# Performance work log

Hardware: AMD Instinct MI355X
Metric: run time of the kernel (lower is better)

Reference implementation:

```python
import jax, jax.numpy as jnp
import numpy as np

N_NODES = 100000
N_EDGES = 1600000
IN_CH = 128
HID = 64
HEADS = 2
OUT_CH = 2
EDGE_DIM = 3
NEG_SLOPE = 0.2
EPS = 1e-16  # PyG softmax denominator epsilon


def gat_conv(x, edge_index, edge_attr, W, We, att_src, att_dst, att_edge, bias, heads, out_ch, concat):
    """Faithful PyG GATConv (edge_dim enabled, eval mode, add_self_loops handled by caller=False here
    since the repo passes raw edge_index; PyG default add_self_loops=True is intentionally mirrored below)."""
    N = x.shape[0]
    src, dst = edge_index[0], edge_index[1]
    H, C = heads, out_ch
    h = (x @ W).reshape(N, H, C)                    # [N,H,C] node projections
    e = (edge_attr @ We).reshape(-1, H, C)          # [E,H,C] edge projections
    a_src = jnp.sum(h * att_src, axis=-1)           # [N,H]
    a_dst = jnp.sum(h * att_dst, axis=-1)           # [N,H]
    alpha = a_src[src] + a_dst[dst] + jnp.sum(e * att_edge, axis=-1)  # [E,H]
    alpha = jax.nn.leaky_relu(alpha, NEG_SLOPE)
    # segment softmax over incoming edges of each dst node
    amax = jax.ops.segment_max(alpha, dst, num_segments=N)            # [N,H]
    amax = jnp.where(jnp.isfinite(amax), amax, 0.0)
    alpha = jnp.exp(alpha - amax[dst])
    denom = jax.ops.segment_sum(alpha, dst, num_segments=N)           # [N,H]
    alpha = alpha / (denom[dst] + EPS)
    msg = h[src] * alpha[:, :, None]                                  # [E,H,C]
    out = jax.ops.segment_sum(msg, dst, num_segments=N)               # [N,H,C]
    if concat:
        out = out.reshape(N, H * C)
    else:
        out = out.mean(axis=1)
    return out + bias


def add_self_loops(edge_index, edge_attr, n):
    loops = jnp.arange(n, dtype=edge_index.dtype)
    ei = jnp.concatenate([edge_index, jnp.stack([loops, loops])], axis=1)
    ea = jnp.concatenate([edge_attr, jnp.zeros((n, edge_attr.shape[1]), edge_attr.dtype)], axis=0)
    return ei, ea


def setup_inputs() -> dict:
    key = jax.random.key(0)
    ks = jax.random.split(key, 16)
    s = 0.1
    x = jax.random.normal(ks[0], (N_NODES, IN_CH), jnp.float32)
    edge_index = jax.random.randint(ks[1], (2, N_EDGES), 0, N_NODES, jnp.int64 if jax.config.jax_enable_x64 else jnp.int32)
    edge_feat = jax.random.normal(ks[2], (N_EDGES, EDGE_DIM), jnp.float32)
    HC = HEADS * HID
    return {
        "x": x, "edge_index": edge_index, "edge_feat": edge_feat,
        "W1": jax.random.normal(ks[3], (IN_CH, HC), jnp.float32) * s,
        "We1": jax.random.normal(ks[4], (EDGE_DIM, HC), jnp.float32) * s,
        "as1": jax.random.normal(ks[5], (1, HEADS, HID), jnp.float32) * s,
        "ad1": jax.random.normal(ks[6], (1, HEADS, HID), jnp.float32) * s,
        "ae1": jax.random.normal(ks[7], (1, HEADS, HID), jnp.float32) * s,
        "b1": jnp.zeros((HC,), jnp.float32),
        "W2": jax.random.normal(ks[8], (HC, OUT_CH), jnp.float32) * s,
        "We2": jax.random.normal(ks[9], (EDGE_DIM, OUT_CH), jnp.float32) * s,
        "as2": jax.random.normal(ks[10], (1, 1, OUT_CH), jnp.float32) * s,
        "ad2": jax.random.normal(ks[11], (1, 1, OUT_CH), jnp.float32) * s,
        "ae2": jax.random.normal(ks[12], (1, 1, OUT_CH), jnp.float32) * s,
        "b2": jnp.zeros((OUT_CH,), jnp.float32),
    }


def reference(x, edge_index, edge_feat, W1, We1, as1, ad1, ae1, b1, W2, We2, as2, ad2, ae2, b2):
    # eval mode: F.dropout is identity
    ei, ea = add_self_loops(edge_index, edge_feat, x.shape[0])  # PyG GATConv default add_self_loops=True
    h = gat_conv(x, ei, ea, W1, We1, as1, ad1, ae1, b1, HEADS, HID, concat=True)
    h = jax.nn.elu(h)
    out = gat_conv(h, ei, ea, W2, We2, as2, ad2, ae2, b2, 1, OUT_CH, concat=False)
    return out
```

## Files before the change

kernel.cpp:

```cpp
#include <hip/hip_runtime.h>
#include <hip/hip_bf16.h>

#define NN 100000
#define NE 1600000
#define NEG_SLOPE 0.2f
#define GEPS 1e-16f
#define WSHIFT 4.0f

#define HB 64
#define EB (NE / HB)
#define HPASS 4
#define HBIN 25000
#define HBW (HBIN / 2)
#define CAPS ((size_t)(NE + 8 * NN))

#define SRCMASK 0x1FFFFu

#define HIST_BLKS (HB * HPASS)
#define GEMM_BLKS ((NN + 127) / 128)

#define EDGE_BLKS ((NE / 4 + 255) / 256)
#define FILL_BLKS ((NN + 255) / 256)
#define NB_DEG    ((NN + 255) / 256)

typedef __attribute__((ext_vector_type(8))) short short8;
typedef __attribute__((ext_vector_type(4))) float f32x4;
typedef __attribute__((ext_vector_type(2))) float f32x2;
typedef __attribute__((ext_vector_type(2))) _Float16 h2v;

__device__ __forceinline__ unsigned short f2b(float f) {
  unsigned u = __float_as_uint(f);
  u += 0x7fffu + ((u >> 16) & 1u);
  return (unsigned short)(u >> 16);
}
__device__ __forceinline__ unsigned short f2h(float f) {
  _Float16 h = (_Float16)f;
  return __builtin_bit_cast(unsigned short, h);
}
__device__ __forceinline__ float h2f(unsigned short u) {
  return (float)__builtin_bit_cast(_Float16, u);
}
__device__ __forceinline__ unsigned pkh2(float lo, float hi) {
  return (unsigned)f2h(lo) | ((unsigned)f2h(hi) << 16);
}
__device__ __forceinline__ float dot2h(unsigned a, unsigned b, float c) {
  return __builtin_amdgcn_fdot2(__builtin_bit_cast(h2v, a), __builtin_bit_cast(h2v, b), c, false);
}
__device__ __forceinline__ unsigned permb(unsigned s0, unsigned s1, int sel) {
  return __builtin_amdgcn_perm(s0, s1, sel);
}
__device__ __forceinline__ unsigned pkSE(int src, float ez) {
  return (unsigned)src | ((unsigned)(f2h(ez) >> 1) << 17);
}
__device__ __forceinline__ float unpkEZ(unsigned y) {
  return h2f((unsigned short)((y >> 17) << 1));
}
__device__ __forceinline__ float4 ntld4(const float4* p) {
  f32x4 v = __builtin_nontemporal_load((const f32x4*)p);
  float4 r; r.x = v.x; r.y = v.y; r.z = v.z; r.w = v.w; return r;
}
__device__ __forceinline__ float2 ntld2(const float2* p) {
  f32x2 v = __builtin_nontemporal_load((const f32x2*)p);
  float2 r; r.x = v.x; r.y = v.y; return r;
}
#define HSEL_LO 0x05040100
#define HSEL_HI 0x07060302
#define ONE2    0x3C003C00u
#define EZPAD   (-60000.0f)

__global__ void k_prep(const float* __restrict__ We1, const float* __restrict__ ae1,
                       const float* __restrict__ We2, const float* __restrict__ ae2,
                       const float* __restrict__ W1, const float* __restrict__ as1,
                       const float* __restrict__ ad1,
                       float* __restrict__ q, float4* __restrict__ pq) {
  int t = threadIdx.x;
  if (t < 6) {
    int d = t >> 1, hh = t & 1;
    float s = 0.f;
    for (int c = 0; c < 64; ++c) s += We1[d * 128 + hh * 64 + c] * ae1[hh * 64 + c];
    q[t] = s;
  } else if (t < 9) {
    int d = t - 6;
    q[8 + d] = We2[d * 2 + 0] * ae2[0] + We2[d * 2 + 1] * ae2[1];
  }
  if (t < 128) {
    float s0 = 0.f, s1 = 0.f, d0 = 0.f, d1 = 0.f;
    for (int c = 0; c < 64; ++c) {
      float w0 = W1[t * 128 + c], w1 = W1[t * 128 + 64 + c];
      s0 += w0 * as1[c];      s1 += w1 * as1[64 + c];
      d0 += w0 * ad1[c];      d1 += w1 * ad1[64 + c];
    }
    pq[t] = make_float4(s0, s1, d0, d1);
  }
}

__global__ __launch_bounds__(512, 4) void k_gh(
    const int* __restrict__ ei, unsigned short* __restrict__ off16,
    unsigned short* __restrict__ rank,
    const float* __restrict__ x, const float* __restrict__ W,
    const float4* __restrict__ pq, unsigned short* __restrict__ h1b,
    float* __restrict__ a1s, float* __restrict__ a1d) {
  __shared__ union SM {
    struct { unsigned short xa[128 * 128]; unsigned short wt[128 * 128]; } g;
    unsigned cnt[HBW];
  } sm;
  int t = threadIdx.x;

  if (blockIdx.x < HIST_BLKS) {
    int b = blockIdx.x >> 2;
    int pass = blockIdx.x & 3;
    int base = pass * HBIN;
    for (int i = t; i < HBW; i += 512) sm.cnt[i] = 0;
    __syncthreads();
    const int* dsts = &ei[NE + b * EB];
    for (int i = t * 4; i < EB; i += 2048) {
      int4 d = *(const int4*)&dsts[i];
      int dv[4] = {d.x, d.y, d.z, d.w};
#pragma unroll
      for (int j = 0; j < 4; ++j) {
        int rel = dv[j] - base;
        if ((unsigned)rel < (unsigned)HBIN) {
          unsigned sh = (unsigned)(rel & 1) << 4;
          unsigned old = atomicAdd(&sm.cnt[rel >> 1], 1u << sh);
          rank[b * EB + i + j] = (unsigned short)((old >> sh) & 0xffffu);
        }
      }
    }
    __syncthreads();
    unsigned short* dp = &off16[(size_t)b * NN + base];
    for (int i = t; i < HBW; i += 512) *(unsigned*)&dp[i * 2] = sm.cnt[i];
    return;
  }

  unsigned short* xa = sm.g.xa;
  unsigned short* wt = sm.g.wt;
  int row0 = (int)(blockIdx.x - HIST_BLKS) * 128;

  {
    int kr = t >> 2, n0 = (t & 3) * 32;
    const float* wp = &W[kr * 128 + n0];
    int cb = kr >> 3, klo = kr & 7;
#pragma unroll
    for (int j = 0; j < 8; ++j) {
      float4 v = *(const float4*)&wp[j * 4];
      int n = n0 + j * 4;
      wt[(n + 0) * 128 + ((cb ^ ((n + 0) & 15)) * 8) + klo] = f2b(v.x);
      wt[(n + 1) * 128 + ((cb ^ ((n + 1) & 15)) * 8) + klo] = f2b(v.y);
      wt[(n + 2) * 128 + ((cb ^ ((n + 2) & 15)) * 8) + klo] = f2b(v.z);
      wt[(n + 3) * 128 + ((cb ^ ((n + 3) & 15)) * 8) + klo] = f2b(v.w);
    }
  }
  {
    int lrow = t >> 2, qq = t & 3;
    int grow = row0 + lrow; if (grow >= NN) grow = NN - 1;
    const float* xp = &x[(size_t)grow * 128 + qq * 32];
    const float4* pqp = &pq[qq * 32];
    float ps0 = 0.f, ps1 = 0.f, pd0 = 0.f, pd1 = 0.f;
    int sw = lrow & 15;
#pragma unroll
    for (int j = 0; j < 4; ++j) {
      float4 u = *(const float4*)&xp[j * 8];
      float4 v = *(const float4*)&xp[j * 8 + 4];
      float xs[8] = {u.x, u.y, u.z, u.w, v.x, v.y, v.z, v.w};
      short8 sv;
#pragma unroll
      for (int e = 0; e < 8; ++e) {
        float4 pv = pqp[j * 8 + e];
        ps0 += xs[e] * pv.x; ps1 += xs[e] * pv.y;
        pd0 += xs[e] * pv.z; pd1 += xs[e] * pv.w;
        sv[e] = (short)f2b(xs[e]);
      }
      int c = qq * 4 + j;
      *(short8*)&xa[lrow * 128 + ((c ^ sw) * 8)] = sv;
    }
    ps0 += __shfl_xor(ps0, 1); ps0 += __shfl_xor(ps0, 2);
    ps1 += __shfl_xor(ps1, 1); ps1 += __shfl_xor(ps1, 2);
    pd0 += __shfl_xor(pd0, 1); pd0 += __shfl_xor(pd0, 2);
    pd1 += __shfl_xor(pd1, 1); pd1 += __shfl_xor(pd1, 2);
    if (qq == 0) {
      *(float2*)&a1s[grow * 2] = make_float2(ps0, ps1);
      *(float2*)&a1d[grow * 2] = make_float2(pd0, pd1);
    }
  }
  __syncthreads();

  int lane = t & 63, w = t >> 6;
  int m = lane & 15, quad = lane >> 4;
  int wm = (w & 1) * 64, wn = (w >> 1) * 32;
  f32x4 acc[4][2];
#pragma unroll
  for (int mi = 0; mi < 4; ++mi)
#pragma unroll
    for (int ni = 0; ni < 2; ++ni) acc[mi][ni] = (f32x4)(0.f);

#pragma unroll
  for (int kk = 0; kk < 4; ++kk) {
    int c = kk * 4 + quad;
    int co = (c ^ m) * 8;
    short8 a[4], b[2];
#pragma unroll
    for (int mi = 0; mi < 4; ++mi)
      a[mi] = *(const short8*)&xa[(wm + mi * 16 + m) * 128 + co];
#pragma unroll
    for (int ni = 0; ni < 2; ++ni)
      b[ni] = *(const short8*)&wt[(wn + ni * 16 + m) * 128 + co];
#pragma unroll
    for (int mi = 0; mi < 4; ++mi)
#pragma unroll
      for (int ni = 0; ni < 2; ++ni)
        acc[mi][ni] = __builtin_amdgcn_mfma_f32_16x16x32_bf16(a[mi], b[ni], acc[mi][ni], 0, 0, 0);
  }
#pragma unroll
  for (int mi = 0; mi < 4; ++mi)
#pragma unroll
    for (int r = 0; r < 4; ++r) {
      int grow = row0 + wm + mi * 16 + quad * 4 + r;
      if (grow >= NN) grow = NN - 1;
#pragma unroll
      for (int ni = 0; ni < 2; ++ni)
        h1b[(size_t)grow * 128 + wn + ni * 16 + m] = f2h(acc[mi][ni][r]);
    }
}

__device__ __forceinline__ int padlen(int d) { return (d + 8) & ~7; }

__global__ void k_degscan(unsigned short* __restrict__ off16, int* __restrict__ deg,
                          int* __restrict__ bsum) {
  __shared__ int lds[256];
  int t = threadIdx.x;
  int n = blockIdx.x * 256 + t;
  int run = 0;
  if (n < NN) {
    for (int b = 0; b < HB; ++b) {
      size_t idx = (size_t)b * NN + n;
      int c = off16[idx];
      off16[idx] = (unsigned short)run;
      run += c;
    }
    deg[n] = run;
  }
  lds[t] = (n < NN) ? padlen(run) : 0;
  __syncthreads();
  for (int o = 128; o > 0; o >>= 1) { if (t < o) lds[t] += lds[t + o]; __syncthreads(); }
  if (t == 0) bsum[blockIdx.x] = lds[0];
}

__global__ void k_scan3(const int* __restrict__ deg, const int* __restrict__ bsum,
                        int* __restrict__ rowptr) {
  __shared__ int lds[256];
  __shared__ int bb;
  int t = threadIdx.x;
  int lim = blockIdx.x * 4;
  int a = 0;
  for (int i = t; i < lim; i += 256) a += bsum[i];
  lds[t] = a; __syncthreads();
  for (int o = 128; o > 0; o >>= 1) { if (t < o) lds[t] += lds[t + o]; __syncthreads(); }
  if (t == 0) bb = lds[0];
  __syncthreads();
  int base = blockIdx.x * 1024 + t * 4;
  int v[4]; int s = 0;
  for (int j = 0; j < 4; ++j) { int i = base + j; v[j] = (i < NN) ? padlen(deg[i]) : 0; s += v[j]; }
  lds[t] = s; __syncthreads();
  for (int o = 1; o < 256; o <<= 1) {
    int u = (t >= o) ? lds[t - o] : 0;
    __syncthreads();
    lds[t] += u;
    __syncthreads();
  }
  int excl = lds[t] - s + bb;
  for (int j = 0; j < 4; ++j) {
    int i = base + j;
    if (i <= NN) rowptr[i] = excl;
    excl += v[j];
  }
}

__global__ void k_scatter(const int* __restrict__ ei, const float* __restrict__ ef,
                          const float* __restrict__ a1s, const float* __restrict__ a1d,
                          const float* __restrict__ q, const int* __restrict__ rowptr,
                          const int* __restrict__ deg,
                          const unsigned short* __restrict__ rank,
                          const unsigned short* __restrict__ off16,
                          float2* __restrict__ cpk1) {
  int bid = blockIdx.x;
  if (bid < EDGE_BLKS) {
    int t4 = bid * 256 + threadIdx.x;
    if (t4 >= NE / 4) return;
    int e0 = t4 * 4;
    int hb = e0 / EB;
    const unsigned short* offp = &off16[(size_t)hb * NN];
    int4 ss = *(const int4*)&ei[e0];
    int4 dd = *(const int4*)&ei[NE + e0];
    ushort4 rk = *(const ushort4*)&rank[e0];
    float4 fA = *(const float4*)&ef[e0 * 3];
    float4 fB = *(const float4*)&ef[e0 * 3 + 4];
    float4 fC = *(const float4*)&ef[e0 * 3 + 8];
    float f[4][3] = {{fA.x, fA.y, fA.z}, {fA.w, fB.x, fB.y},
                     {fB.z, fB.w, fC.x}, {fC.y, fC.z, fC.w}};
    int src[4] = {ss.x, ss.y, ss.z, ss.w};
    int dst[4] = {dd.x, dd.y, dd.z, dd.w};
    int rnk[4] = {rk.x, rk.y, rk.z, rk.w};
#pragma unroll
    for (int j = 0; j < 4; ++j) {
      float e0h = f[j][0] * q[0] + f[j][1] * q[2] + f[j][2] * q[4];
      float e1h = f[j][0] * q[1] + f[j][1] * q[3] + f[j][2] * q[5];
      float ez  = f[j][0] * q[8] + f[j][1] * q[9] + f[j][2] * q[10];
      float al0 = a1s[src[j] * 2] + a1d[dst[j] * 2] + e0h;
      float al1 = a1s[src[j] * 2 + 1] + a1d[dst[j] * 2 + 1] + e1h;
      al0 = al0 > 0.f ? al0 : NEG_SLOPE * al0;
      al1 = al1 > 0.f ? al1 : NEG_SLOPE * al1;
      int pos = rowptr[dst[j]] + 1 + (int)offp[dst[j]] + rnk[j];
      cpk1[pos] = make_float2(
          __uint_as_float(pkh2(__expf(al0 - WSHIFT), __expf(al1 - WSHIFT))),
          __uint_as_float(pkSE(src[j], ez)));
    }
  } else {
    int n = (bid - EDGE_BLKS) * 256 + threadIdx.x;
    if (n >= NN) return;
    int s0 = rowptr[n];
    int d = deg[n];
    int pl = padlen(d);
    float2 sv = *(const float2*)&a1s[n * 2];
    float2 dv = *(const float2*)&a1d[n * 2];
    float al0 = sv.x + dv.x;
    float al1 = sv.y + dv.y;
    al0 = al0 > 0.f ? al0 : NEG_SLOPE * al0;
    al1 = al1 > 0.f ? al1 : NEG_SLOPE * al1;
    cpk1[s0] = make_float2(
        __uint_as_float(pkh2(__expf(al0 - WSHIFT), __expf(al1 - WSHIFT))),
        __uint_as_float(pkSE(n, 0.f)));
    float2 pad = make_float2(0.f, __uint_as_float(pkSE(n, EZPAD)));
    for (int k = 1 + d; k < pl; ++k) cpk1[s0 + k] = pad;
  }
}

__global__ __launch_bounds__(256) void k_agg1(const unsigned short* __restrict__ h1b,
                                              const int* __restrict__ rowptr,
                                              const float2* __restrict__ cpk1,
                                              const float* __restrict__ b1,
                                              const float* __restrict__ W2,
                                              const float* __restrict__ as2,
                                              const float* __restrict__ ad2,
                                              float4* __restrict__ nd) {
  int n = (int)((blockIdx.x * 256 + threadIdx.x) >> 6);
  int lane = threadIdx.x & 63;
  if (n >= NN) return;
  int s0 = rowptr[n], s1 = rowptr[n + 1];
  int g = lane >> 4;
  int lp = lane & 15;
  int wsel = (lp >= 8) ? HSEL_HI : HSEL_LO;

  float acc[8];
#pragma unroll
  for (int j = 0; j < 8; ++j) acc[j] = 0.f;
  float den = 0.f;

  int i = s0;
  for (; i + 16 <= s1; i += 16) {
    const float4* pp = (const float4*)(cpk1 + i + 4 * g);
    float4 p01 = ntld4(pp);
    float4 p23 = ntld4(pp + 1);
    uint4 vA = *((const uint4*)(h1b + ((size_t)(__float_as_uint(p01.y) & SRCMASK) << 7)) + lp);
    uint4 vB = *((const uint4*)(h1b + ((size_t)(__float_as_uint(p01.w) & SRCMASK) << 7)) + lp);
    uint4 vC = *((const uint4*)(h1b + ((size_t)(__float_as_uint(p23.y) & SRCMASK) << 7)) + lp);
    uint4 vD = *((const uint4*)(h1b + ((size_t)(__float_as_uint(p23.w) & SRCMASK) << 7)) + lp);
    unsigned wAB = permb(__float_as_uint(p01.z), __float_as_uint(p01.x), wsel);
    unsigned wCD = permb(__float_as_uint(p23.z), __float_as_uint(p23.x), wsel);
    den = dot2h(wAB, ONE2, den);
    den = dot2h(wCD, ONE2, den);
    acc[0] = dot2h(permb(vB.x, vA.x, HSEL_LO), wAB, acc[0]);
    acc[1] = dot2h(permb(vB.x, vA.x, HSEL_HI), wAB, acc[1]);
    acc[2] = dot2h(permb(vB.y, vA.y, HSEL_LO), wAB, acc[2]);
    acc[3] = dot2h(permb(vB.y, vA.y, HSEL_HI), wAB, acc[3]);
    acc[4] = dot2h(permb(vB.z, vA.z, HSEL_LO), wAB, acc[4]);
    acc[5] = dot2h(permb(vB.z, vA.z, HSEL_HI), wAB, acc[5]);
    acc[6] = dot2h(permb(vB.w, vA.w, HSEL_LO), wAB, acc[6]);
    acc[7] = dot2h(permb(vB.w, vA.w, HSEL_HI), wAB, acc[7]);
    acc[0] = dot2h(permb(vD.x, vC.x, HSEL_LO), wCD, acc[0]);
    acc[1] = dot2h(permb(vD.x, vC.x, HSEL_HI), wCD, acc[1]);
    acc[2] = dot2h(permb(vD.y, vC.y, HSEL_LO), wCD, acc[2]);
    acc[3] = dot2h(permb(vD.y, vC.y, HSEL_HI), wCD, acc[3]);
    acc[4] = dot2h(permb(vD.z, vC.z, HSEL_LO), wCD, acc[4]);
    acc[5] = dot2h(permb(vD.z, vC.z, HSEL_HI), wCD, acc[5]);
    acc[6] = dot2h(permb(vD.w, vC.w, HSEL_LO), wCD, acc[6]);
    acc[7] = dot2h(permb(vD.w, vC.w, HSEL_HI), wCD, acc[7]);
  }
  if (i < s1) {
    float4 p = ntld4((const float4*)(cpk1 + i + 2 * g));
    uint4 vA = *((const uint4*)(h1b + ((size_t)(__float_as_uint(p.y) & SRCMASK) << 7)) + lp);
    uint4 vB = *((const uint4*)(h1b + ((size_t)(__float_as_uint(p.w) & SRCMASK) << 7)) + lp);
    unsigned wAB = permb(__float_as_uint(p.z), __float_as_uint(p.x), wsel);
    den = dot2h(wAB, ONE2, den);
    acc[0] = dot2h(permb(vB.x, vA.x, HSEL_LO), wAB, acc[0]);
    acc[1] = dot2h(permb(vB.x, vA.x, HSEL_HI), wAB, acc[1]);
    acc[2] = dot2h(permb(vB.y, vA.y, HSEL_LO), wAB, acc[2]);
    acc[3] = dot2h(permb(vB.y, vA.y, HSEL_HI), wAB, acc[3]);
    acc[4] = dot2h(permb(vB.z, vA.z, HSEL_LO), wAB, acc[4]);
    acc[5] = dot2h(permb(vB.z, vA.z, HSEL_HI), wAB, acc[5]);
    acc[6] = dot2h(permb(vB.w, vA.w, HSEL_LO), wAB, acc[6]);
    acc[7] = dot2h(permb(vB.w, vA.w, HSEL_HI), wAB, acc[7]);
  }
#pragma unroll
  for (int o = 16; o <= 32; o <<= 1) {
    den += __shfl_xor(den, o);
#pragma unroll
    for (int j = 0; j < 8; ++j) acc[j] += __shfl_xor(acc[j], o);
  }
  float4 bA = *(const float4*)&b1[lp * 8];
  float4 bB = *(const float4*)&b1[lp * 8 + 4];
  float bb[8] = {bA.x, bA.y, bA.z, bA.w, bB.x, bB.y, bB.z, bB.w};
  float inv = 1.f / (den + GEPS);
  float r[8];
#pragma unroll
  for (int j = 0; j < 8; ++j) {
    float v = acc[j] * inv + bb[j];
    r[j] = v > 0.f ? v : __expf(v) - 1.f;
  }
  float4 wA = *(const float4*)&W2[lp * 16];
  float4 wB = *(const float4*)&W2[lp * 16 + 4];
  float4 wC = *(const float4*)&W2[lp * 16 + 8];
  float4 wD = *(const float4*)&W2[lp * 16 + 12];
  float p20 = r[0] * wA.x + r[1] * wA.z + r[2] * wB.x + r[3] * wB.z
            + r[4] * wC.x + r[5] * wC.z + r[6] * wD.x + r[7] * wD.z;
  float p21 = r[0] * wA.y + r[1] * wA.w + r[2] * wB.y + r[3] * wB.w
            + r[4] * wC.y + r[5] * wC.w + r[6] * wD.y + r[7] * wD.w;
#pragma unroll
  for (int o = 1; o <= 8; o <<= 1) { p20 += __shfl_xor(p20, o); p21 += __shfl_xor(p21, o); }
  if (lane == 0) {
    float4 v;
    v.x = p20; v.y = p21;
    v.z = p20 * as2[0] + p21 * as2[1];
    v.w = p20 * ad2[0] + p21 * ad2[1];
    nd[n] = v;
  }
}

__global__ __launch_bounds__(256) void k_agg2(const int* __restrict__ rowptr,
                                              const float2* __restrict__ cpk1,
                                              const float4* __restrict__ nd,
                                              const float* __restrict__ b2,
                                              float* __restrict__ out) {
  int wid = (int)((blockIdx.x * 256 + threadIdx.x) >> 6);
  int lane = threadIdx.x & 63;
  int g = lane >> 4, lp = lane & 15;
  int n = wid * 4 + g;
  if (n >= NN) return;
  int s0 = rowptr[n], s1 = rowptr[n + 1];
  float adn = nd[n].w;
  float den = 0.f, acc0 = 0.f, acc1 = 0.f;
  for (int i = s0 + lp; i < s1; i += 16) {
    float2 pk = ntld2(&cpk1[i]);
    unsigned y = __float_as_uint(pk.y);
    int s = (int)(y & SRCMASK);
    float ezv = unpkEZ(y);
    float4 ns = nd[s];
    float v = ns.z + adn + ezv;
    v = v > 0.f ? v : NEG_SLOPE * v;
    float p = __expf(v);
    den += p;
    acc0 += p * ns.x;
    acc1 += p * ns.y;
  }
#pragma unroll
  for (int o = 1; o <= 8; o <<= 1) {
    den += __shfl_xor(den, o);
    acc0 += __shfl_xor(acc0, o);
    acc1 += __shfl_xor(acc1, o);
  }
  if (lp == 0) {
    float2 r;
    r.x = acc0 / (den + GEPS) + b2[0];
    r.y = acc1 / (den + GEPS) + b2[1];
    *(float2*)&out[n * 2] = r;
  }
}

extern "C" void kernel_launch(void* const* d_in, const int* in_sizes, int n_in,
                              void* d_out, int out_size, void* d_ws, size_t ws_size,
                              hipStream_t stream) {
  (void)in_sizes; (void)n_in; (void)out_size; (void)ws_size;
  const float* x   = (const float*)d_in[0];
  const int*   ei  = (const int*)d_in[1];
  const float* ef  = (const float*)d_in[2];
  const float* W1  = (const float*)d_in[3];
  const float* We1 = (const float*)d_in[4];
  const float* as1 = (const float*)d_in[5];
  const float* ad1 = (const float*)d_in[6];
  const float* ae1 = (const float*)d_in[7];
  const float* b1  = (const float*)d_in[8];
  const float* W2  = (const float*)d_in[9];
  const float* We2 = (const float*)d_in[10];
  const float* as2 = (const float*)d_in[11];
  const float* ad2 = (const float*)d_in[12];
  const float* ae2 = (const float*)d_in[13];
  const float* b2  = (const float*)d_in[14];
  float* out = (float*)d_out;

  char* w = (char*)d_ws;
  auto alloc = [&](size_t bytes) -> char* {
    char* p = w; w += (bytes + 255) & ~(size_t)255; return p;
  };
  unsigned short* h1b = (unsigned short*)alloc((size_t)NN * 128 * 2);
  float*  a1s    = (float*)alloc((size_t)NN * 2 * 4);
  float*  a1d    = (float*)alloc((size_t)NN * 2 * 4);
  float4* nd     = (float4*)alloc((size_t)NN * 16);
  float*  q      = (float*)alloc(64);
  float4* pq     = (float4*)alloc(128 * 16);
  int*    deg    = (int*)alloc((size_t)NN * 4);
  int*    rowptr = (int*)alloc((size_t)(NN + 1) * 4);
  unsigned short* rank  = (unsigned short*)alloc((size_t)NE * 2);
  unsigned short* off16 = (unsigned short*)alloc((size_t)HB * NN * 2);
  int*    bsum   = (int*)alloc(512 * 4);
  float2* cpk1   = (float2*)alloc(CAPS * 8);

  const int NB_SCAN = (NN + 1023) / 1024;

  hipLaunchKernelGGL(k_prep, dim3(1), dim3(128), 0, stream,
                     We1, ae1, We2, ae2, W1, as1, ad1, q, pq);
  hipLaunchKernelGGL(k_gh, dim3(HIST_BLKS + GEMM_BLKS), dim3(512), 0, stream,
                     ei, off16, rank, x, W1, pq, h1b, a1s, a1d);
  hipLaunchKernelGGL(k_degscan, dim3(NB_DEG), dim3(256), 0, stream, off16, deg, bsum);
  hipLaunchKernelGGL(k_scan3, dim3(NB_SCAN), dim3(256), 0, stream, deg, bsum, rowptr);
  hipLaunchKernelGGL(k_scatter, dim3(EDGE_BLKS + FILL_BLKS), dim3(256), 0, stream,
                     ei, ef, a1s, a1d, q, rowptr, deg, rank, off16, cpk1);
  hipLaunchKernelGGL(k_agg1, dim3((NN * 64 + 255) / 256), dim3(256), 0, stream,
                     h1b, rowptr, cpk1, b1, W2, as2, ad2, nd);
  hipLaunchKernelGGL(k_agg2, dim3(((NN + 3) / 4 * 64 + 255) / 256), dim3(256), 0, stream,
                     rowptr, cpk1, nd, b2, out);
}
```

Before: 332.7 us.

## Fuse degree scan, scatter and aggregation stages into one cooperative persistent kernel

Folds the five post-GEMM kernels (degree scan, rowptr scan, CSR scatter, layer-1 and layer-2 aggregation) into a single cooperative kernel. The kernel loops over work units with grid-stride and separates stages with grid.sync, falling back to separate launches if the cooperative launch fails. The goal is to remove per-kernel launch gaps and drain/fill bubbles between stages. In exchange, each grid-wide barrier has a cost, occupancy is capped by launch bounds, and a fixed persistent grid may balance the irregular aggregation work worse than the original large grids.

```diff
diff --git a/kernel.cpp b/kernel.cpp
--- a/kernel.cpp
+++ b/kernel.cpp
@@ -1,5 +1,7 @@
 #include <hip/hip_runtime.h>
 #include <hip/hip_bf16.h>
+#include <hip/hip_cooperative_groups.h>
+namespace cg = cooperative_groups;
 
 #define NN 100000
 #define NE 1600000
@@ -21,7 +23,12 @@
 
 #define EDGE_BLKS ((NE / 4 + 255) / 256)
 #define FILL_BLKS ((NN + 255) / 256)
+#define SCAT_UNITS (EDGE_BLKS + FILL_BLKS)
 #define NB_DEG    ((NN + 255) / 256)
+#define NB_SCAN3  ((NN + 1023) / 1024)
+#define AGG1_UNITS ((NN + 3) / 4)
+#define AGG2_UNITS ((NN + 15) / 16)
+#define NUM_CU 256
 
 typedef __attribute__((ext_vector_type(8))) short short8;
 typedef __attribute__((ext_vector_type(4))) float f32x4;
@@ -67,6 +74,8 @@
 #define HSEL_HI 0x07060302
 #define ONE2    0x3C003C00u
 #define EZPAD   (-60000.0f)
+
+__device__ __forceinline__ int padlen(int d) { return (d + 8) & ~7; }
 
 __global__ void k_prep(const float* __restrict__ We1, const float* __restrict__ ae1,
                        const float* __restrict__ We2, const float* __restrict__ ae2,
@@ -222,13 +231,9 @@
     }
 }
 
-__device__ __forceinline__ int padlen(int d) { return (d + 8) & ~7; }
-
-__global__ void k_degscan(unsigned short* __restrict__ off16, int* __restrict__ deg,
-                          int* __restrict__ bsum) {
-  __shared__ int lds[256];
-  int t = threadIdx.x;
-  int n = blockIdx.x * 256 + t;
+__device__ __forceinline__ void d_degscan(int u, int t, unsigned short* off16,
+                                          int* deg, int* bsum, int* lds) {
+  int n = u * 256 + t;
   int run = 0;
   if (n < NN) {
     for (int b = 0; b < HB; ++b) {
@@ -242,49 +247,45 @@
   lds[t] = (n < NN) ? padlen(run) : 0;
   __syncthreads();
   for (int o = 128; o > 0; o >>= 1) { if (t < o) lds[t] += lds[t + o]; __syncthreads(); }
-  if (t == 0) bsum[blockIdx.x] = lds[0];
-}
-
-__global__ void k_scan3(const int* __restrict__ deg, const int* __restrict__ bsum,
-                        int* __restrict__ rowptr) {
-  __shared__ int lds[256];
-  __shared__ int bb;
-  int t = threadIdx.x;
-  int lim = blockIdx.x * 4;
+  if (t == 0) bsum[u] = lds[0];
+  __syncthreads();
+}
+
+__device__ __forceinline__ void d_scan3(int u, int t, const int* deg, const int* bsum,
+                                        int* rowptr, int* lds) {
+  int lim = u * 4;
   int a = 0;
   for (int i = t; i < lim; i += 256) a += bsum[i];
   lds[t] = a; __syncthreads();
   for (int o = 128; o > 0; o >>= 1) { if (t < o) lds[t] += lds[t + o]; __syncthreads(); }
-  if (t == 0) bb = lds[0];
+  int bbv = lds[0];
   __syncthreads();
-  int base = blockIdx.x * 1024 + t * 4;
+  int base = u * 1024 + t * 4;
   int v[4]; int s = 0;
   for (int j = 0; j < 4; ++j) { int i = base + j; v[j] = (i < NN) ? padlen(deg[i]) : 0; s += v[j]; }
   lds[t] = s; __syncthreads();
   for (int o = 1; o < 256; o <<= 1) {
-    int u = (t >= o) ? lds[t - o] : 0;
+    int uu = (t >= o) ? lds[t - o] : 0;
     __syncthreads();
-    lds[t] += u;
+    lds[t] += uu;
     __syncthreads();
   }
-  int excl = lds[t] - s + bb;
+  int excl = lds[t] - s + bbv;
   for (int j = 0; j < 4; ++j) {
     int i = base + j;
     if (i <= NN) rowptr[i] = excl;
     excl += v[j];
   }
-}
-
-__global__ void k_scatter(const int* __restrict__ ei, const float* __restrict__ ef,
-                          const float* __restrict__ a1s, const float* __restrict__ a1d,
-                          const float* __restrict__ q, const int* __restrict__ rowptr,
-                          const int* __restrict__ deg,
-                          const unsigned short* __restrict__ rank,
-                          const unsigned short* __restrict__ off16,
-                          float2* __restrict__ cpk1) {
-  int bid = blockIdx.x;
-  if (bid < EDGE_BLKS) {
-    int t4 = bid * 256 + threadIdx.x;
+  __syncthreads();
+}
+
+__device__ __forceinline__ void d_scat(int u, int t, const int* ei, const float* ef,
+                                       const float* a1s, const float* a1d,
+                                       const float* q, const int* rowptr,
+                                       const int* deg, const unsigned short* rank,
+                                       const unsigned short* off16, float2* cpk1) {
+  if (u < EDGE_BLKS) {
+    int t4 = u * 256 + t;
     if (t4 >= NE / 4) return;
     int e0 = t4 * 4;
     int hb = e0 / EB;
@@ -315,7 +316,7 @@
           __uint_as_float(pkSE(src[j], ez)));
     }
   } else {
-    int n = (bid - EDGE_BLKS) * 256 + threadIdx.x;
+    int n = (u - EDGE_BLKS) * 256 + t;
     if (n >= NN) return;
     int s0 = rowptr[n];
     int d = deg[n];
@@ -334,27 +335,21 @@
   }
 }
 
-__global__ __launch_bounds__(256) void k_agg1(const unsigned short* __restrict__ h1b,
-                                              const int* __restrict__ rowptr,
-                                              const float2* __restrict__ cpk1,
-                                              const float* __restrict__ b1,
-                                              const float* __restrict__ W2,
-                                              const float* __restrict__ as2,
-                                              const float* __restrict__ ad2,
-                                              float4* __restrict__ nd) {
-  int n = (int)((blockIdx.x * 256 + threadIdx.x) >> 6);
-  int lane = threadIdx.x & 63;
+__device__ __forceinline__ void d_agg1(int u, int t, const unsigned short* h1b,
+                                       const int* rowptr, const float2* cpk1,
+                                       const float* b1, const float* W2,
+                                       const float* as2, const float* ad2, float4* nd) {
+  int n = u * 4 + (t >> 6);
+  int lane = t & 63;
   if (n >= NN) return;
   int s0 = rowptr[n], s1 = rowptr[n + 1];
   int g = lane >> 4;
   int lp = lane & 15;
   int wsel = (lp >= 8) ? HSEL_HI : HSEL_LO;
-
   float acc[8];
 #pragma unroll
   for (int j = 0; j < 8; ++j) acc[j] = 0.f;
   float den = 0.f;
-
   int i = s0;
   for (; i + 16 <= s1; i += 16) {
     const float4* pp = (const float4*)(cpk1 + i + 4 * g);
@@ -408,12 +403,12 @@
   }
   float4 bA = *(const float4*)&b1[lp * 8];
   float4 bB = *(const float4*)&b1[lp * 8 + 4];
-  float bb[8] = {bA.x, bA.y, bA.z, bA.w, bB.x, bB.y, bB.z, bB.w};
+  float bbv[8] = {bA.x, bA.y, bA.z, bA.w, bB.x, bB.y, bB.z, bB.w};
   float inv = 1.f / (den + GEPS);
   float r[8];
 #pragma unroll
   for (int j = 0; j < 8; ++j) {
-    float v = acc[j] * inv + bb[j];
+    float v = acc[j] * inv + bbv[j];
     r[j] = v > 0.f ? v : __expf(v) - 1.f;
   }
   float4 wA = *(const float4*)&W2[lp * 16];
@@ -435,13 +430,11 @@
   }
 }
 
-__global__ __launch_bounds__(256) void k_agg2(const int* __restrict__ rowptr,
-                                              const float2* __restrict__ cpk1,
-                                              const float4* __restrict__ nd,
-                                              const float* __restrict__ b2,
-                                              float* __restrict__ out) {
-  int wid = (int)((blockIdx.x * 256 + threadIdx.x) >> 6);
-  int lane = threadIdx.x & 63;
+__device__ __forceinline__ void d_agg2(int u, int t, const int* rowptr,
+                                       const float2* cpk1, const float4* nd,
+                                       const float* b2, float* out) {
+  int wid = u * 4 + (t >> 6);
+  int lane = t & 63;
   int g = lane >> 4, lp = lane & 15;
   int n = wid * 4 + g;
   if (n >= NN) return;
@@ -473,6 +466,78 @@
     r.y = acc1 / (den + GEPS) + b2[1];
     *(float2*)&out[n * 2] = r;
   }
+}
+
+__global__ __launch_bounds__(256, 8) void k_tail(
+    unsigned short* __restrict__ off16, int* __restrict__ deg, int* __restrict__ bsum,
+    const int* __restrict__ ei, const float* __restrict__ ef,
+    const float* __restrict__ a1s, const float* __restrict__ a1d,
+    const float* __restrict__ q, int* __restrict__ rowptr,
+    const unsigned short* __restrict__ rank, float2* __restrict__ cpk1,
+    const unsigned short* __restrict__ h1b, const float* __restrict__ b1,
+    const float* __restrict__ W2, const float* __restrict__ as2,
+    const float* __restrict__ ad2, float4* __restrict__ nd,
+    const float* __restrict__ b2, float* __restrict__ out) {
+  cg::grid_group grid = cg::this_grid();
+  __shared__ int lds[256];
+  int t = threadIdx.x;
+
+  for (int u = blockIdx.x; u < NB_DEG; u += gridDim.x)
+    d_degscan(u, t, off16, deg, bsum, lds);
+  __threadfence();
+  grid.sync();
+
+  for (int u = blockIdx.x; u < NB_SCAN3; u += gridDim.x)
+    d_scan3(u, t, deg, bsum, rowptr, lds);
+  __threadfence();
+  grid.sync();
+
+  for (int u = blockIdx.x; u < SCAT_UNITS; u += gridDim.x)
+    d_scat(u, t, ei, ef, a1s, a1d, q, rowptr, deg, rank, off16, cpk1);
+  __threadfence();
+  grid.sync();
+
+  for (int u = blockIdx.x; u < AGG1_UNITS; u += gridDim.x)
+    d_agg1(u, t, h1b, rowptr, cpk1, b1, W2, as2, ad2, nd);
+  __threadfence();
+  grid.sync();
+
+  for (int u = blockIdx.x; u < AGG2_UNITS; u += gridDim.x)
+    d_agg2(u, t, rowptr, cpk1, nd, b2, out);
+}
+
+__global__ __launch_bounds__(256) void k_degscan(unsigned short* __restrict__ off16,
+                                                 int* __restrict__ deg,
+                                                 int* __restrict__ bsum) {
+  __shared__ int lds[256];
+  d_degscan(blockIdx.x, threadIdx.x, off16, deg, bsum, lds);
+}
+__global__ __launch_bounds__(256) void k_scan3(const int* __restrict__ deg,
+                                               const int* __restrict__ bsum,
+                                               int* __restrict__ rowptr) {
+  __shared__ int lds[256];
+  d_scan3(blockIdx.x, threadIdx.x, deg, bsum, rowptr, lds);
+}
+__global__ __launch_bounds__(256) void k_scatter(
+    const int* __restrict__ ei, const float* __restrict__ ef,
+    const float* __restrict__ a1s, const float* __restrict__ a1d,
+    const float* __restrict__ q, const int* __restrict__ rowptr,
+    const int* __restrict__ deg, const unsigned short* __restrict__ rank,
+    const unsigned short* __restrict__ off16, float2* __restrict__ cpk1) {
+  d_scat(blockIdx.x, threadIdx.x, ei, ef, a1s, a1d, q, rowptr, deg, rank, off16, cpk1);
+}
+__global__ __launch_bounds__(256) void k_agg1(
+    const unsigned short* __restrict__ h1b, const int* __restrict__ rowptr,
+    const float2* __restrict__ cpk1, const float* __restrict__ b1,
+    const float* __restrict__ W2, const float* __restrict__ as2,
+    const float* __restrict__ ad2, float4* __restrict__ nd) {
+  d_agg1(blockIdx.x, threadIdx.x, h1b, rowptr, cpk1, b1, W2, as2, ad2, nd);
+}
+__global__ __launch_bounds__(256) void k_agg2(
+    const int* __restrict__ rowptr, const float2* __restrict__ cpk1,
+    const float4* __restrict__ nd, const float* __restrict__ b2,
+    float* __restrict__ out) {
+  d_agg2(blockIdx.x, threadIdx.x, rowptr, cpk1, nd, b2, out);
 }
 
 extern "C" void kernel_launch(void* const* d_in, const int* in_sizes, int n_in,
@@ -513,18 +578,37 @@
   int*    bsum   = (int*)alloc(512 * 4);
   float2* cpk1   = (float2*)alloc(CAPS * 8);
 
-  const int NB_SCAN = (NN + 1023) / 1024;
-
   hipLaunchKernelGGL(k_prep, dim3(1), dim3(128), 0, stream,
                      We1, ae1, We2, ae2, W1, as1, ad1, q, pq);
   hipLaunchKernelGGL(k_gh, dim3(HIST_BLKS + GEMM_BLKS), dim3(512), 0, stream,
                      ei, off16, rank, x, W1, pq, h1b, a1s, a1d);
-  hipLaunchKernelGGL(k_degscan, dim3(NB_DEG), dim3(256), 0, stream, off16, deg, bsum);
-  hipLaunchKernelGGL(k_scan3, dim3(NB_SCAN), dim3(256), 0, stream, deg, bsum, rowptr);
-  hipLaunchKernelGGL(k_scatter, dim3(EDGE_BLKS + FILL_BLKS), dim3(256), 0, stream,
-                     ei, ef, a1s, a1d, q, rowptr, deg, rank, off16, cpk1);
-  hipLaunchKernelGGL(k_agg1, dim3((NN * 64 + 255) / 256), dim3(256), 0, stream,
-                     h1b, rowptr, cpk1, b1, W2, as2, ad2, nd);
-  hipLaunchKernelGGL(k_agg2, dim3(((NN + 3) / 4 * 64 + 255) / 256), dim3(256), 0, stream,
-                     rowptr, cpk1, nd, b2, out);
-}
+
+  bool coop_ok = false;
+  {
+    int occ = 0;
+    hipError_t e1 = hipOccupancyMaxActiveBlocksPerMultiprocessor(
+        &occ, (const void*)k_tail, 256, 0);
+    if (e1 == hipSuccess && occ > 0) {
+      long long blocks = (long long)occ * NUM_CU;
+      if (blocks > SCAT_UNITS) blocks = SCAT_UNITS;
+      void* args[] = {(void*)&off16, (void*)&deg, (void*)&bsum, (void*)&ei, (void*)&ef,
+                      (void*)&a1s, (void*)&a1d, (void*)&q, (void*)&rowptr, (void*)&rank,
+                      (void*)&cpk1, (void*)&h1b, (void*)&b1, (void*)&W2, (void*)&as2,
+                      (void*)&ad2, (void*)&nd, (void*)&b2, (void*)&out};
+      hipError_t e2 = hipLaunchCooperativeKernel((const void*)k_tail,
+                                                 dim3((unsigned)blocks), dim3(256),
+                                                 args, 0, stream);
+      coop_ok = (e2 == hipSuccess);
+    }
+  }
+  if (!coop_ok) {
+    hipLaunchKernelGGL(k_degscan, dim3(NB_DEG), dim3(256), 0, stream, off16, deg, bsum);
+    hipLaunchKernelGGL(k_scan3, dim3(NB_SCAN3), dim3(256), 0, stream, deg, bsum, rowptr);
+    hipLaunchKernelGGL(k_scatter, dim3(SCAT_UNITS), dim3(256), 0, stream,
+                       ei, ef, a1s, a1d, q, rowptr, deg, rank, off16, cpk1);
+    hipLaunchKernelGGL(k_agg1, dim3(AGG1_UNITS), dim3(256), 0, stream,
+                       h1b, rowptr, cpk1, b1, W2, as2, ad2, nd);
+    hipLaunchKernelGGL(k_agg2, dim3(AGG2_UNITS), dim3(256), 0, stream,
+                       rowptr, cpk1, nd, b2, out);
+  }
+}
```

New measurement: 1.255 ms. 3.77x slower.
